# Kernel optimization log

Measured on AMD Instinct MI355X. Metric: run time of the kernel, lower is better.

The kernel has to match this reference:

```python
import jax, jax.numpy as jnp
import numpy as np

MASK_VALUE = -1000000.0  # matches torch source's value=-1000000.0


def setup_inputs() -> dict:
    key = jax.random.key(0)
    kq, kk, kv, kl = jax.random.split(key, 4)
    B, S, D = 64, 1024, 64
    q = jax.random.normal(kq, (B, S, D), dtype=jnp.float32)
    k = jax.random.normal(kk, (B, S, D), dtype=jnp.float32)
    v = jax.random.normal(kv, (B, S, D), dtype=jnp.float32)
    valid_lens = jax.random.randint(kl, (B,), 0, S, dtype=jnp.int32)
    return {"q": q, "k": k, "v": v, "valid_lens": valid_lens}


def reference(q, k, v, valid_lens):
    # scores: [B, Sq, Sk]
    d = q.shape[-1]
    scores = jnp.einsum("bqd,bkd->bqk", q, k) / jnp.sqrt(jnp.float32(d))
    # 1-D valid_lens broadcast over the query dim (torch repeat_interleave branch)
    Sk = k.shape[1]
    mask = jnp.arange(Sk, dtype=jnp.int32)[None, None, :] < valid_lens[:, None, None]
    scores = jnp.where(mask, scores, MASK_VALUE)
    attn = jax.nn.softmax(scores, axis=-1)
    # dropout p=0.0 -> identity (eval-mode reference)
    return jnp.einsum("bqk,bkd->bqd", attn, v)
```

## Files before the change

### kernel.cpp

```cpp
#include <hip/hip_runtime.h>
#include <math.h>


#define BATCH 64
#define SEQ   1024
#define DIM   64
#define BQ    64
#define BC    64
#define NKT   (SEQ / BC)
#define LSTR  72
#define QSCALE 0.18033688011112442f
#define MASKED -1.0e6f
#define THR    8.0f

typedef __attribute__((ext_vector_type(8))) short bf16x8;
typedef __attribute__((ext_vector_type(4))) float f32x4;

__device__ __forceinline__ uint pack2_trunc(float lo, float hi) {
    return __builtin_amdgcn_perm(__float_as_uint(hi), __float_as_uint(lo), 0x07060302);
}
__device__ __forceinline__ ushort f2bf_rne(float x) {
    uint u = __float_as_uint(x);
    return (ushort)((u + 0x7fffu + ((u >> 16) & 1u)) >> 16);
}

__global__ __launch_bounds__(256, 4) void attn_mfma_flash4(
    const float* __restrict__ q, const float* __restrict__ k,
    const float* __restrict__ v, const int* __restrict__ valid_lens,
    float* __restrict__ out)
{
    __shared__ ushort Ks[BC * LSTR];
    __shared__ ushort Vt[DIM * LSTR];

    const int t    = threadIdx.x;
    const int wave = t >> 6;
    const int wl   = t & 63;
    const int QD   = wl >> 4;
    const int li   = wl & 15;
    const int b    = blockIdx.x & 63;
    const int q0   = (blockIdx.x >> 6) * BQ;
    const int vl   = valid_lens[b];

    const size_t boff = (size_t)b * SEQ * DIM;

    bf16x8 qb[2];
    {
        const float* qrow = q + boff + (size_t)(q0 + wave * 16 + li) * DIM + QD * 8;
        #pragma unroll
        for (int kc = 0; kc < 2; kc++) {
            float4 a = *(const float4*)(qrow + kc * 32);
            float4 c = *(const float4*)(qrow + kc * 32 + 4);
            union { bf16x8 v; ushort u[8]; } tmp;
            tmp.u[0] = f2bf_rne(a.x * QSCALE);
            tmp.u[1] = f2bf_rne(a.y * QSCALE);
            tmp.u[2] = f2bf_rne(a.z * QSCALE);
            tmp.u[3] = f2bf_rne(a.w * QSCALE);
            tmp.u[4] = f2bf_rne(c.x * QSCALE);
            tmp.u[5] = f2bf_rne(c.y * QSCALE);
            tmp.u[6] = f2bf_rne(c.z * QSCALE);
            tmp.u[7] = f2bf_rne(c.w * QSCALE);
            qb[kc] = tmp.v;
        }
    }

    const int it_max = (vl == 0) ? NKT : ((vl + BC - 1) >> 6);

    float4 kf[4];
    float  vf[2][8];

    auto load_tile = [&](int it) {
        const float4* kg = (const float4*)(k + boff + (size_t)it * BC * DIM);
        #pragma unroll
        for (int i = 0; i < 4; i++) kf[i] = kg[t + 256 * i];
        const float* vgf = v + boff + (size_t)it * BC * DIM;
        #pragma unroll
        for (int i = 0; i < 2; i++) {
            int slot = t + 256 * i;
            int d = slot & 63, ko = slot >> 6;
            int kb = (ko >> 2) * 16 + (ko & 3) * 4;
            #pragma unroll
            for (int j = 0; j < 8; j++) {
                int kk = kb + ((j >> 2) << 5) + (j & 3);
                vf[i][j] = vgf[(size_t)kk * DIM + d];
            }
        }
    };

    auto stage = [&]() {
        #pragma unroll
        for (int i = 0; i < 4; i++) {
            int idx = t + 256 * i;
            int row = idx >> 4, c4 = idx & 15;
            uint2 w;
            w.x = pack2_trunc(kf[i].x, kf[i].y);
            w.y = pack2_trunc(kf[i].z, kf[i].w);
            *(uint2*)&Ks[row * LSTR + c4 * 4] = w;
        }
        #pragma unroll
        for (int i = 0; i < 2; i++) {
            int slot = t + 256 * i;
            int d = slot & 63, ko = slot >> 6;
            uint4 w;
            w.x = pack2_trunc(vf[i][0], vf[i][1]);
            w.y = pack2_trunc(vf[i][2], vf[i][3]);
            w.z = pack2_trunc(vf[i][4], vf[i][5]);
            w.w = pack2_trunc(vf[i][6], vf[i][7]);
            *(uint4*)&Vt[d * LSTR + ko * 8] = w;
        }
    };

    float m_run = -INFINITY, l_run = 0.f;
    f32x4 acc[4];
    #pragma unroll
    for (int dt = 0; dt < 4; dt++) acc[dt] = (f32x4){0.f, 0.f, 0.f, 0.f};

    load_tile(0);

    for (int it = 0; it < it_max; it++) {
        __builtin_amdgcn_sched_barrier(0);
        __builtin_amdgcn_s_barrier();
        __builtin_amdgcn_sched_barrier(0);

        stage();
        if (it + 1 < it_max) load_tile(it + 1);

        __builtin_amdgcn_sched_barrier(0);
        asm volatile("s_waitcnt lgkmcnt(0)" ::: "memory");
        __builtin_amdgcn_s_barrier();
        __builtin_amdgcn_sched_barrier(0);

        f32x4 sc[4];
        #pragma unroll
        for (int kt = 0; kt < 4; kt++) {
            bf16x8 ka0 = *(const bf16x8*)&Ks[(kt * 16 + li) * LSTR + QD * 8];
            bf16x8 ka1 = *(const bf16x8*)&Ks[(kt * 16 + li) * LSTR + 32 + QD * 8];
            f32x4 c = (f32x4){0.f, 0.f, 0.f, 0.f};
            c = __builtin_amdgcn_mfma_f32_16x16x32_bf16(ka0, qb[0], c, 0, 0, 0);
            c = __builtin_amdgcn_mfma_f32_16x16x32_bf16(ka1, qb[1], c, 0, 0, 0);
            sc[kt] = c;
        }

        const int kbase = it * BC;
        if (kbase + BC > vl) {
            #pragma unroll
            for (int kt = 0; kt < 4; kt++)
                #pragma unroll
                for (int r = 0; r < 4; r++) {
                    int key = kbase + kt * 16 + QD * 4 + r;
                    if (key >= vl) sc[kt][r] = MASKED;
                }
        }

        float mt = -INFINITY;
        #pragma unroll
        for (int kt = 0; kt < 4; kt++)
            #pragma unroll
            for (int r = 0; r < 4; r++) mt = fmaxf(mt, sc[kt][r]);
        mt = fmaxf(mt, __shfl_xor(mt, 16, 64));
        mt = fmaxf(mt, __shfl_xor(mt, 32, 64));

        if (!__all(mt - m_run <= THR)) {
            float mn = fmaxf(m_run, mt);
            float alpha = exp2f(m_run - mn);
            m_run = mn;
            l_run *= alpha;
            float a0 = __shfl(alpha, QD * 4 + 0, 64);
            float a1 = __shfl(alpha, QD * 4 + 1, 64);
            float a2 = __shfl(alpha, QD * 4 + 2, 64);
            float a3 = __shfl(alpha, QD * 4 + 3, 64);
            #pragma unroll
            for (int dt = 0; dt < 4; dt++) {
                acc[dt][0] *= a0; acc[dt][1] *= a1;
                acc[dt][2] *= a2; acc[dt][3] *= a3;
            }
        }

        float ls = 0.f;
        union { bf16x8 v; uint u[4]; } pa0u, pa1u;
        {
            float p00 = exp2f(sc[0][0] - m_run), p01 = exp2f(sc[0][1] - m_run);
            float p02 = exp2f(sc[0][2] - m_run), p03 = exp2f(sc[0][3] - m_run);
            float p10 = exp2f(sc[1][0] - m_run), p11 = exp2f(sc[1][1] - m_run);
            float p12 = exp2f(sc[1][2] - m_run), p13 = exp2f(sc[1][3] - m_run);
            float p20 = exp2f(sc[2][0] - m_run), p21 = exp2f(sc[2][1] - m_run);
            float p22 = exp2f(sc[2][2] - m_run), p23 = exp2f(sc[2][3] - m_run);
            float p30 = exp2f(sc[3][0] - m_run), p31 = exp2f(sc[3][1] - m_run);
            float p32 = exp2f(sc[3][2] - m_run), p33 = exp2f(sc[3][3] - m_run);
            ls = ((p00 + p01) + (p02 + p03)) + ((p10 + p11) + (p12 + p13))
               + ((p20 + p21) + (p22 + p23)) + ((p30 + p31) + (p32 + p33));
            pa0u.u[0] = pack2_trunc(p00, p01);
            pa0u.u[1] = pack2_trunc(p02, p03);
            pa0u.u[2] = pack2_trunc(p20, p21);
            pa0u.u[3] = pack2_trunc(p22, p23);
            pa1u.u[0] = pack2_trunc(p10, p11);
            pa1u.u[1] = pack2_trunc(p12, p13);
            pa1u.u[2] = pack2_trunc(p30, p31);
            pa1u.u[3] = pack2_trunc(p32, p33);
        }
        ls += __shfl_xor(ls, 16, 64);
        ls += __shfl_xor(ls, 32, 64);
        l_run += ls;

        #pragma unroll
        for (int dt = 0; dt < 4; dt++) {
            bf16x8 vb0 = *(const bf16x8*)&Vt[(dt * 16 + li) * LSTR + QD * 8];
            bf16x8 vb1 = *(const bf16x8*)&Vt[(dt * 16 + li) * LSTR + 32 + QD * 8];
            acc[dt] = __builtin_amdgcn_mfma_f32_16x16x32_bf16(pa0u.v, vb0, acc[dt], 0, 0, 0);
            acc[dt] = __builtin_amdgcn_mfma_f32_16x16x32_bf16(pa1u.v, vb1, acc[dt], 0, 0, 0);
        }
    }

    float invl = 1.0f / l_run;
    float i0 = __shfl(invl, QD * 4 + 0, 64);
    float i1 = __shfl(invl, QD * 4 + 1, 64);
    float i2 = __shfl(invl, QD * 4 + 2, 64);
    float i3 = __shfl(invl, QD * 4 + 3, 64);
    float* ob = out + boff + (size_t)q0 * DIM;
    const int rbase = wave * 16 + QD * 4;
    #pragma unroll
    for (int dt = 0; dt < 4; dt++) {
        int col = dt * 16 + li;
        ob[(size_t)(rbase + 0) * DIM + col] = acc[dt][0] * i0;
        ob[(size_t)(rbase + 1) * DIM + col] = acc[dt][1] * i1;
        ob[(size_t)(rbase + 2) * DIM + col] = acc[dt][2] * i2;
        ob[(size_t)(rbase + 3) * DIM + col] = acc[dt][3] * i3;
    }
}

extern "C" void kernel_launch(void* const* d_in, const int* in_sizes, int n_in,
                              void* d_out, int out_size, void* d_ws, size_t ws_size,
                              hipStream_t stream) {
    const float* q = (const float*)d_in[0];
    const float* k = (const float*)d_in[1];
    const float* v = (const float*)d_in[2];
    const int* valid_lens = (const int*)d_in[3];
    float* out = (float*)d_out;

    dim3 grid(BATCH * (SEQ / BQ));
    dim3 block(256);
    attn_mfma_flash4<<<grid, block, 0, stream>>>(q, k, v, valid_lens, out);
}
```

Before: 124.4 us.

## Process two 64-row query tiles per block to reuse staged K/V tiles

Doubles the query rows per block to 128, with each wave holding two independent query sub-tiles, A and B, that share each K/V tile staged in LDS. This halves the global K/V loads and bf16 conversion/staging work per query row. Block-to-batch mapping is rotated per group to spread the uneven valid_lens work across blocks. Grid size halves to 512 blocks and register pressure roughly doubles, which lowers occupancy and reduces the parallelism available for load balancing.

```diff
diff --git a/kernel.cpp b/kernel.cpp
--- a/kernel.cpp
+++ b/kernel.cpp
@@ -5,7 +5,7 @@
 #define BATCH 64
 #define SEQ   1024
 #define DIM   64
-#define BQ    64
+#define BQ    128
 #define BC    64
 #define NKT   (SEQ / BC)
 #define LSTR  72
@@ -24,7 +24,7 @@
     return (ushort)((u + 0x7fffu + ((u >> 16) & 1u)) >> 16);
 }
 
-__global__ __launch_bounds__(256, 4) void attn_mfma_flash4(
+__global__ __launch_bounds__(256, 1) void attn_mfma_flash5(
     const float* __restrict__ q, const float* __restrict__ k,
     const float* __restrict__ v, const int* __restrict__ valid_lens,
     float* __restrict__ out)
@@ -37,29 +37,35 @@
     const int wl   = t & 63;
     const int QD   = wl >> 4;
     const int li   = wl & 15;
-    const int b    = blockIdx.x & 63;
-    const int q0   = (blockIdx.x >> 6) * BQ;
+    const int g    = blockIdx.x;
+    const int grp  = g >> 6;
+    const int b    = ((g & 63) + grp) & 63;
+    const int q0   = grp * BQ;
     const int vl   = valid_lens[b];
 
     const size_t boff = (size_t)b * SEQ * DIM;
 
-    bf16x8 qb[2];
+    bf16x8 qbA[2], qbB[2];
     {
-        const float* qrow = q + boff + (size_t)(q0 + wave * 16 + li) * DIM + QD * 8;
-        #pragma unroll
-        for (int kc = 0; kc < 2; kc++) {
-            float4 a = *(const float4*)(qrow + kc * 32);
-            float4 c = *(const float4*)(qrow + kc * 32 + 4);
-            union { bf16x8 v; ushort u[8]; } tmp;
-            tmp.u[0] = f2bf_rne(a.x * QSCALE);
-            tmp.u[1] = f2bf_rne(a.y * QSCALE);
-            tmp.u[2] = f2bf_rne(a.z * QSCALE);
-            tmp.u[3] = f2bf_rne(a.w * QSCALE);
-            tmp.u[4] = f2bf_rne(c.x * QSCALE);
-            tmp.u[5] = f2bf_rne(c.y * QSCALE);
-            tmp.u[6] = f2bf_rne(c.z * QSCALE);
-            tmp.u[7] = f2bf_rne(c.w * QSCALE);
-            qb[kc] = tmp.v;
+        #pragma unroll
+        for (int half = 0; half < 2; half++) {
+            const float* qrow = q + boff
+                + (size_t)(q0 + half * 64 + wave * 16 + li) * DIM + QD * 8;
+            #pragma unroll
+            for (int kc = 0; kc < 2; kc++) {
+                float4 a = *(const float4*)(qrow + kc * 32);
+                float4 c = *(const float4*)(qrow + kc * 32 + 4);
+                union { bf16x8 v; ushort u[8]; } tmp;
+                tmp.u[0] = f2bf_rne(a.x * QSCALE);
+                tmp.u[1] = f2bf_rne(a.y * QSCALE);
+                tmp.u[2] = f2bf_rne(a.z * QSCALE);
+                tmp.u[3] = f2bf_rne(a.w * QSCALE);
+                tmp.u[4] = f2bf_rne(c.x * QSCALE);
+                tmp.u[5] = f2bf_rne(c.y * QSCALE);
+                tmp.u[6] = f2bf_rne(c.z * QSCALE);
+                tmp.u[7] = f2bf_rne(c.w * QSCALE);
+                if (half == 0) qbA[kc] = tmp.v; else qbB[kc] = tmp.v;
+            }
         }
     }
 
@@ -109,10 +115,13 @@
         }
     };
 
-    float m_run = -INFINITY, l_run = 0.f;
-    f32x4 acc[4];
+    float mA = -INFINITY, lA = 0.f, mB = -INFINITY, lB = 0.f;
+    f32x4 accA[4], accB[4];
     #pragma unroll
-    for (int dt = 0; dt < 4; dt++) acc[dt] = (f32x4){0.f, 0.f, 0.f, 0.f};
+    for (int dt = 0; dt < 4; dt++) {
+        accA[dt] = (f32x4){0.f, 0.f, 0.f, 0.f};
+        accB[dt] = (f32x4){0.f, 0.f, 0.f, 0.f};
+    }
 
     load_tile(0);
 
@@ -129,15 +138,19 @@
         __builtin_amdgcn_s_barrier();
         __builtin_amdgcn_sched_barrier(0);
 
-        f32x4 sc[4];
+        f32x4 scA[4], scB[4];
         #pragma unroll
         for (int kt = 0; kt < 4; kt++) {
             bf16x8 ka0 = *(const bf16x8*)&Ks[(kt * 16 + li) * LSTR + QD * 8];
             bf16x8 ka1 = *(const bf16x8*)&Ks[(kt * 16 + li) * LSTR + 32 + QD * 8];
-            f32x4 c = (f32x4){0.f, 0.f, 0.f, 0.f};
-            c = __builtin_amdgcn_mfma_f32_16x16x32_bf16(ka0, qb[0], c, 0, 0, 0);
-            c = __builtin_amdgcn_mfma_f32_16x16x32_bf16(ka1, qb[1], c, 0, 0, 0);
-            sc[kt] = c;
+            f32x4 cA = (f32x4){0.f, 0.f, 0.f, 0.f};
+            cA = __builtin_amdgcn_mfma_f32_16x16x32_bf16(ka0, qbA[0], cA, 0, 0, 0);
+            cA = __builtin_amdgcn_mfma_f32_16x16x32_bf16(ka1, qbA[1], cA, 0, 0, 0);
+            scA[kt] = cA;
+            f32x4 cB = (f32x4){0.f, 0.f, 0.f, 0.f};
+            cB = __builtin_amdgcn_mfma_f32_16x16x32_bf16(ka0, qbB[0], cB, 0, 0, 0);
+            cB = __builtin_amdgcn_mfma_f32_16x16x32_bf16(ka1, qbB[1], cB, 0, 0, 0);
+            scB[kt] = cB;
         }
 
         const int kbase = it * BC;
@@ -147,83 +160,136 @@
                 #pragma unroll
                 for (int r = 0; r < 4; r++) {
                     int key = kbase + kt * 16 + QD * 4 + r;
-                    if (key >= vl) sc[kt][r] = MASKED;
+                    if (key >= vl) { scA[kt][r] = MASKED; scB[kt][r] = MASKED; }
                 }
         }
 
-        float mt = -INFINITY;
-        #pragma unroll
-        for (int kt = 0; kt < 4; kt++)
-            #pragma unroll
-            for (int r = 0; r < 4; r++) mt = fmaxf(mt, sc[kt][r]);
-        mt = fmaxf(mt, __shfl_xor(mt, 16, 64));
-        mt = fmaxf(mt, __shfl_xor(mt, 32, 64));
-
-        if (!__all(mt - m_run <= THR)) {
-            float mn = fmaxf(m_run, mt);
-            float alpha = exp2f(m_run - mn);
-            m_run = mn;
-            l_run *= alpha;
-            float a0 = __shfl(alpha, QD * 4 + 0, 64);
-            float a1 = __shfl(alpha, QD * 4 + 1, 64);
-            float a2 = __shfl(alpha, QD * 4 + 2, 64);
-            float a3 = __shfl(alpha, QD * 4 + 3, 64);
-            #pragma unroll
-            for (int dt = 0; dt < 4; dt++) {
-                acc[dt][0] *= a0; acc[dt][1] *= a1;
-                acc[dt][2] *= a2; acc[dt][3] *= a3;
+        union { bf16x8 v; uint u[4]; } pA0, pA1, pB0, pB1;
+        {
+            float mt = -INFINITY;
+            #pragma unroll
+            for (int kt = 0; kt < 4; kt++)
+                #pragma unroll
+                for (int r = 0; r < 4; r++) mt = fmaxf(mt, scA[kt][r]);
+            mt = fmaxf(mt, __shfl_xor(mt, 16, 64));
+            mt = fmaxf(mt, __shfl_xor(mt, 32, 64));
+            if (!__all(mt - mA <= THR)) {
+                float mn = fmaxf(mA, mt);
+                float alpha = exp2f(mA - mn);
+                mA = mn; lA *= alpha;
+                float a0 = __shfl(alpha, QD * 4 + 0, 64);
+                float a1 = __shfl(alpha, QD * 4 + 1, 64);
+                float a2 = __shfl(alpha, QD * 4 + 2, 64);
+                float a3 = __shfl(alpha, QD * 4 + 3, 64);
+                #pragma unroll
+                for (int dt = 0; dt < 4; dt++) {
+                    accA[dt][0] *= a0; accA[dt][1] *= a1;
+                    accA[dt][2] *= a2; accA[dt][3] *= a3;
+                }
             }
-        }
-
-        float ls = 0.f;
-        union { bf16x8 v; uint u[4]; } pa0u, pa1u;
+            float p00 = exp2f(scA[0][0] - mA), p01 = exp2f(scA[0][1] - mA);
+            float p02 = exp2f(scA[0][2] - mA), p03 = exp2f(scA[0][3] - mA);
+            float p10 = exp2f(scA[1][0] - mA), p11 = exp2f(scA[1][1] - mA);
+            float p12 = exp2f(scA[1][2] - mA), p13 = exp2f(scA[1][3] - mA);
+            float p20 = exp2f(scA[2][0] - mA), p21 = exp2f(scA[2][1] - mA);
+            float p22 = exp2f(scA[2][2] - mA), p23 = exp2f(scA[2][3] - mA);
+            float p30 = exp2f(scA[3][0] - mA), p31 = exp2f(scA[3][1] - mA);
+            float p32 = exp2f(scA[3][2] - mA), p33 = exp2f(scA[3][3] - mA);
+            float ls = ((p00 + p01) + (p02 + p03)) + ((p10 + p11) + (p12 + p13))
+                     + ((p20 + p21) + (p22 + p23)) + ((p30 + p31) + (p32 + p33));
+            pA0.u[0] = pack2_trunc(p00, p01); pA0.u[1] = pack2_trunc(p02, p03);
+            pA0.u[2] = pack2_trunc(p20, p21); pA0.u[3] = pack2_trunc(p22, p23);
+            pA1.u[0] = pack2_trunc(p10, p11); pA1.u[1] = pack2_trunc(p12, p13);
+            pA1.u[2] = pack2_trunc(p30, p31); pA1.u[3] = pack2_trunc(p32, p33);
+            ls += __shfl_xor(ls, 16, 64);
+            ls += __shfl_xor(ls, 32, 64);
+            lA += ls;
+        }
         {
-            float p00 = exp2f(sc[0][0] - m_run), p01 = exp2f(sc[0][1] - m_run);
-            float p02 = exp2f(sc[0][2] - m_run), p03 = exp2f(sc[0][3] - m_run);
-            float p10 = exp2f(sc[1][0] - m_run), p11 = exp2f(sc[1][1] - m_run);
-            float p12 = exp2f(sc[1][2] - m_run), p13 = exp2f(sc[1][3] - m_run);
-            float p20 = exp2f(sc[2][0] - m_run), p21 = exp2f(sc[2][1] - m_run);
-            float p22 = exp2f(sc[2][2] - m_run), p23 = exp2f(sc[2][3] - m_run);
-            float p30 = exp2f(sc[3][0] - m_run), p31 = exp2f(sc[3][1] - m_run);
-            float p32 = exp2f(sc[3][2] - m_run), p33 = exp2f(sc[3][3] - m_run);
-            ls = ((p00 + p01) + (p02 + p03)) + ((p10 + p11) + (p12 + p13))
-               + ((p20 + p21) + (p22 + p23)) + ((p30 + p31) + (p32 + p33));
-            pa0u.u[0] = pack2_trunc(p00, p01);
-            pa0u.u[1] = pack2_trunc(p02, p03);
-            pa0u.u[2] = pack2_trunc(p20, p21);
-            pa0u.u[3] = pack2_trunc(p22, p23);
-            pa1u.u[0] = pack2_trunc(p10, p11);
-            pa1u.u[1] = pack2_trunc(p12, p13);
-            pa1u.u[2] = pack2_trunc(p30, p31);
-            pa1u.u[3] = pack2_trunc(p32, p33);
-        }
-        ls += __shfl_xor(ls, 16, 64);
-        ls += __shfl_xor(ls, 32, 64);
-        l_run += ls;
+            float mt = -INFINITY;
+            #pragma unroll
+            for (int kt = 0; kt < 4; kt++)
+                #pragma unroll
+                for (int r = 0; r < 4; r++) mt = fmaxf(mt, scB[kt][r]);
+            mt = fmaxf(mt, __shfl_xor(mt, 16, 64));
+            mt = fmaxf(mt, __shfl_xor(mt, 32, 64));
+            if (!__all(mt - mB <= THR)) {
+                float mn = fmaxf(mB, mt);
+                float alpha = exp2f(mB - mn);
+                mB = mn; lB *= alpha;
+                float a0 = __shfl(alpha, QD * 4 + 0, 64);
+                float a1 = __shfl(alpha, QD * 4 + 1, 64);
+                float a2 = __shfl(alpha, QD * 4 + 2, 64);
+                float a3 = __shfl(alpha, QD * 4 + 3, 64);
+                #pragma unroll
+                for (int dt = 0; dt < 4; dt++) {
+                    accB[dt][0] *= a0; accB[dt][1] *= a1;
+                    accB[dt][2] *= a2; accB[dt][3] *= a3;
+                }
+            }
+            float p00 = exp2f(scB[0][0] - mB), p01 = exp2f(scB[0][1] - mB);
+            float p02 = exp2f(scB[0][2] - mB), p03 = exp2f(scB[0][3] - mB);
+            float p10 = exp2f(scB[1][0] - mB), p11 = exp2f(scB[1][1] - mB);
+            float p12 = exp2f(scB[1][2] - mB), p13 = exp2f(scB[1][3] - mB);
+            float p20 = exp2f(scB[2][0] - mB), p21 = exp2f(scB[2][1] - mB);
+            float p22 = exp2f(scB[2][2] - mB), p23 = exp2f(scB[2][3] - mB);
+            float p30 = exp2f(scB[3][0] - mB), p31 = exp2f(scB[3][1] - mB);
+            float p32 = exp2f(scB[3][2] - mB), p33 = exp2f(scB[3][3] - mB);
+            float ls = ((p00 + p01) + (p02 + p03)) + ((p10 + p11) + (p12 + p13))
+                     + ((p20 + p21) + (p22 + p23)) + ((p30 + p31) + (p32 + p33));
+            pB0.u[0] = pack2_trunc(p00, p01); pB0.u[1] = pack2_trunc(p02, p03);
+            pB0.u[2] = pack2_trunc(p20, p21); pB0.u[3] = pack2_trunc(p22, p23);
+            pB1.u[0] = pack2_trunc(p10, p11); pB1.u[1] = pack2_trunc(p12, p13);
+            pB1.u[2] = pack2_trunc(p30, p31); pB1.u[3] = pack2_trunc(p32, p33);
+            ls += __shfl_xor(ls, 16, 64);
+            ls += __shfl_xor(ls, 32, 64);
+            lB += ls;
+        }
 
         #pragma unroll
         for (int dt = 0; dt < 4; dt++) {
             bf16x8 vb0 = *(const bf16x8*)&Vt[(dt * 16 + li) * LSTR + QD * 8];
             bf16x8 vb1 = *(const bf16x8*)&Vt[(dt * 16 + li) * LSTR + 32 + QD * 8];
-            acc[dt] = __builtin_amdgcn_mfma_f32_16x16x32_bf16(pa0u.v, vb0, acc[dt], 0, 0, 0);
-            acc[dt] = __builtin_amdgcn_mfma_f32_16x16x32_bf16(pa1u.v, vb1, acc[dt], 0, 0, 0);
-        }
-    }
-
-    float invl = 1.0f / l_run;
-    float i0 = __shfl(invl, QD * 4 + 0, 64);
-    float i1 = __shfl(invl, QD * 4 + 1, 64);
-    float i2 = __shfl(invl, QD * 4 + 2, 64);
-    float i3 = __shfl(invl, QD * 4 + 3, 64);
-    float* ob = out + boff + (size_t)q0 * DIM;
-    const int rbase = wave * 16 + QD * 4;
-    #pragma unroll
-    for (int dt = 0; dt < 4; dt++) {
-        int col = dt * 16 + li;
-        ob[(size_t)(rbase + 0) * DIM + col] = acc[dt][0] * i0;
-        ob[(size_t)(rbase + 1) * DIM + col] = acc[dt][1] * i1;
-        ob[(size_t)(rbase + 2) * DIM + col] = acc[dt][2] * i2;
-        ob[(size_t)(rbase + 3) * DIM + col] = acc[dt][3] * i3;
+            accA[dt] = __builtin_amdgcn_mfma_f32_16x16x32_bf16(pA0.v, vb0, accA[dt], 0, 0, 0);
+            accA[dt] = __builtin_amdgcn_mfma_f32_16x16x32_bf16(pA1.v, vb1, accA[dt], 0, 0, 0);
+            accB[dt] = __builtin_amdgcn_mfma_f32_16x16x32_bf16(pB0.v, vb0, accB[dt], 0, 0, 0);
+            accB[dt] = __builtin_amdgcn_mfma_f32_16x16x32_bf16(pB1.v, vb1, accB[dt], 0, 0, 0);
+        }
+    }
+
+    {
+        float invl = 1.0f / lA;
+        float i0 = __shfl(invl, QD * 4 + 0, 64);
+        float i1 = __shfl(invl, QD * 4 + 1, 64);
+        float i2 = __shfl(invl, QD * 4 + 2, 64);
+        float i3 = __shfl(invl, QD * 4 + 3, 64);
+        float* ob = out + boff + (size_t)q0 * DIM;
+        const int rbase = wave * 16 + QD * 4;
+        #pragma unroll
+        for (int dt = 0; dt < 4; dt++) {
+            int col = dt * 16 + li;
+            ob[(size_t)(rbase + 0) * DIM + col] = accA[dt][0] * i0;
+            ob[(size_t)(rbase + 1) * DIM + col] = accA[dt][1] * i1;
+            ob[(size_t)(rbase + 2) * DIM + col] = accA[dt][2] * i2;
+            ob[(size_t)(rbase + 3) * DIM + col] = accA[dt][3] * i3;
+        }
+    }
+    {
+        float invl = 1.0f / lB;
+        float i0 = __shfl(invl, QD * 4 + 0, 64);
+        float i1 = __shfl(invl, QD * 4 + 1, 64);
+        float i2 = __shfl(invl, QD * 4 + 2, 64);
+        float i3 = __shfl(invl, QD * 4 + 3, 64);
+        float* ob = out + boff + (size_t)(q0 + 64) * DIM;
+        const int rbase = wave * 16 + QD * 4;
+        #pragma unroll
+        for (int dt = 0; dt < 4; dt++) {
+            int col = dt * 16 + li;
+            ob[(size_t)(rbase + 0) * DIM + col] = accB[dt][0] * i0;
+            ob[(size_t)(rbase + 1) * DIM + col] = accB[dt][1] * i1;
+            ob[(size_t)(rbase + 2) * DIM + col] = accB[dt][2] * i2;
+            ob[(size_t)(rbase + 3) * DIM + col] = accB[dt][3] * i3;
+        }
     }
 }
 
@@ -238,5 +304,5 @@
 
     dim3 grid(BATCH * (SEQ / BQ));
     dim3 block(256);
-    attn_mfma_flash4<<<grid, block, 0, stream>>>(q, k, v, valid_lens, out);
+    attn_mfma_flash5<<<grid, block, 0, stream>>>(q, k, v, valid_lens, out);
 }
```

Result: slower. 127.6 us (+2.6%).

## Split key tiles across two wave groups per block and merge partial softmax

Applied to the files above, without the earlier changes.

Each block now runs 512 threads as two groups of four waves. The groups process alternating key tiles for the same 64 queries, each with its own shared-memory K/V buffer, and their partial accumulators and (max, sum) pairs are merged through shared memory at the end. This roughly halves the serial per-block loop length and doubles the waves available to hide latency. Block indices are also rotated so that batches with different valid lengths are spread across the grid. The cost is more LDS per block, an extra merge phase with barriers, and possibly lower occupancy with 512-thread blocks under launch bounds (512,4).

```diff
diff --git a/kernel.cpp b/kernel.cpp
--- a/kernel.cpp
+++ b/kernel.cpp
@@ -12,6 +12,7 @@
 #define QSCALE 0.18033688011112442f
 #define MASKED -1.0e6f
 #define THR    8.0f
+#define KVSZ   (BC * LSTR)
 
 typedef __attribute__((ext_vector_type(8))) short bf16x8;
 typedef __attribute__((ext_vector_type(4))) float f32x4;
@@ -24,28 +25,36 @@
     return (ushort)((u + 0x7fffu + ((u >> 16) & 1u)) >> 16);
 }
 
-__global__ __launch_bounds__(256, 4) void attn_mfma_flash4(
+__global__ __launch_bounds__(512, 4) void attn_dualgrp(
     const float* __restrict__ q, const float* __restrict__ k,
     const float* __restrict__ v, const int* __restrict__ valid_lens,
     float* __restrict__ out)
 {
-    __shared__ ushort Ks[BC * LSTR];
-    __shared__ ushort Vt[DIM * LSTR];
+    __shared__ ushort SB[4 * KVSZ];
 
     const int t    = threadIdx.x;
     const int wave = t >> 6;
+    const int gid  = wave >> 2;
+    const int wg   = wave & 3;
     const int wl   = t & 63;
     const int QD   = wl >> 4;
     const int li   = wl & 15;
-    const int b    = blockIdx.x & 63;
-    const int q0   = (blockIdx.x >> 6) * BQ;
+    const int tg   = t & 255;
+
+    const int g    = blockIdx.x;
+    const int grp  = g >> 6;
+    const int b    = ((g & 63) + grp) & 63;
+    const int q0   = grp * BQ;
     const int vl   = valid_lens[b];
 
     const size_t boff = (size_t)b * SEQ * DIM;
+
+    ushort* Ksg = SB + gid * (2 * KVSZ);
+    ushort* Vtg = Ksg + KVSZ;
 
     bf16x8 qb[2];
     {
-        const float* qrow = q + boff + (size_t)(q0 + wave * 16 + li) * DIM + QD * 8;
+        const float* qrow = q + boff + (size_t)(q0 + wg * 16 + li) * DIM + QD * 8;
         #pragma unroll
         for (int kc = 0; kc < 2; kc++) {
             float4 a = *(const float4*)(qrow + kc * 32);
@@ -63,7 +72,8 @@
         }
     }
 
-    const int it_max = (vl == 0) ? NKT : ((vl + BC - 1) >> 6);
+    const int it_full = (vl == 0) ? NKT : ((vl + BC - 1) >> 6);
+    const int nmax    = (it_full + 1) >> 1;
 
     float4 kf[4];
     float  vf[2][8];
@@ -71,11 +81,11 @@
     auto load_tile = [&](int it) {
         const float4* kg = (const float4*)(k + boff + (size_t)it * BC * DIM);
         #pragma unroll
-        for (int i = 0; i < 4; i++) kf[i] = kg[t + 256 * i];
+        for (int i = 0; i < 4; i++) kf[i] = kg[tg + 256 * i];
         const float* vgf = v + boff + (size_t)it * BC * DIM;
         #pragma unroll
         for (int i = 0; i < 2; i++) {
-            int slot = t + 256 * i;
+            int slot = tg + 256 * i;
             int d = slot & 63, ko = slot >> 6;
             int kb = (ko >> 2) * 16 + (ko & 3) * 4;
             #pragma unroll
@@ -89,141 +99,177 @@
     auto stage = [&]() {
         #pragma unroll
         for (int i = 0; i < 4; i++) {
-            int idx = t + 256 * i;
+            int idx = tg + 256 * i;
             int row = idx >> 4, c4 = idx & 15;
             uint2 w;
             w.x = pack2_trunc(kf[i].x, kf[i].y);
             w.y = pack2_trunc(kf[i].z, kf[i].w);
-            *(uint2*)&Ks[row * LSTR + c4 * 4] = w;
+            *(uint2*)&Ksg[row * LSTR + c4 * 4] = w;
         }
         #pragma unroll
         for (int i = 0; i < 2; i++) {
-            int slot = t + 256 * i;
+            int slot = tg + 256 * i;
             int d = slot & 63, ko = slot >> 6;
             uint4 w;
             w.x = pack2_trunc(vf[i][0], vf[i][1]);
             w.y = pack2_trunc(vf[i][2], vf[i][3]);
             w.z = pack2_trunc(vf[i][4], vf[i][5]);
             w.w = pack2_trunc(vf[i][6], vf[i][7]);
-            *(uint4*)&Vt[d * LSTR + ko * 8] = w;
+            *(uint4*)&Vtg[d * LSTR + ko * 8] = w;
         }
     };
 
-    float m_run = -INFINITY, l_run = 0.f;
+    float m_run = -INFINITY;
+    float l_run = 0.f;
     f32x4 acc[4];
     #pragma unroll
     for (int dt = 0; dt < 4; dt++) acc[dt] = (f32x4){0.f, 0.f, 0.f, 0.f};
 
-    load_tile(0);
-
-    for (int it = 0; it < it_max; it++) {
+    bool act = (gid < it_full);
+    if (act) load_tile(gid);
+
+    for (int j = 0; j < nmax; j++) {
+        const int tile = gid + 2 * j;
+        const bool act_next = (tile + 2) < it_full;
+
         __builtin_amdgcn_sched_barrier(0);
         __builtin_amdgcn_s_barrier();
         __builtin_amdgcn_sched_barrier(0);
 
-        stage();
-        if (it + 1 < it_max) load_tile(it + 1);
+        if (act) stage();
+        if (act_next) load_tile(tile + 2);
 
         __builtin_amdgcn_sched_barrier(0);
         asm volatile("s_waitcnt lgkmcnt(0)" ::: "memory");
         __builtin_amdgcn_s_barrier();
         __builtin_amdgcn_sched_barrier(0);
 
-        f32x4 sc[4];
-        #pragma unroll
-        for (int kt = 0; kt < 4; kt++) {
-            bf16x8 ka0 = *(const bf16x8*)&Ks[(kt * 16 + li) * LSTR + QD * 8];
-            bf16x8 ka1 = *(const bf16x8*)&Ks[(kt * 16 + li) * LSTR + 32 + QD * 8];
-            f32x4 c = (f32x4){0.f, 0.f, 0.f, 0.f};
-            c = __builtin_amdgcn_mfma_f32_16x16x32_bf16(ka0, qb[0], c, 0, 0, 0);
-            c = __builtin_amdgcn_mfma_f32_16x16x32_bf16(ka1, qb[1], c, 0, 0, 0);
-            sc[kt] = c;
-        }
-
-        const int kbase = it * BC;
-        if (kbase + BC > vl) {
+        if (act) {
+            f32x4 sc[4];
+            #pragma unroll
+            for (int kt = 0; kt < 4; kt++) {
+                bf16x8 ka0 = *(const bf16x8*)&Ksg[(kt * 16 + li) * LSTR + QD * 8];
+                bf16x8 ka1 = *(const bf16x8*)&Ksg[(kt * 16 + li) * LSTR + 32 + QD * 8];
+                f32x4 c = (f32x4){0.f, 0.f, 0.f, 0.f};
+                c = __builtin_amdgcn_mfma_f32_16x16x32_bf16(ka0, qb[0], c, 0, 0, 0);
+                c = __builtin_amdgcn_mfma_f32_16x16x32_bf16(ka1, qb[1], c, 0, 0, 0);
+                sc[kt] = c;
+            }
+
+            const int kbase = tile * BC;
+            if (kbase + BC > vl) {
+                #pragma unroll
+                for (int kt = 0; kt < 4; kt++)
+                    #pragma unroll
+                    for (int r = 0; r < 4; r++) {
+                        int key = kbase + kt * 16 + QD * 4 + r;
+                        if (key >= vl) sc[kt][r] = MASKED;
+                    }
+            }
+
+            float mt = -INFINITY;
             #pragma unroll
             for (int kt = 0; kt < 4; kt++)
                 #pragma unroll
-                for (int r = 0; r < 4; r++) {
-                    int key = kbase + kt * 16 + QD * 4 + r;
-                    if (key >= vl) sc[kt][r] = MASKED;
+                for (int r = 0; r < 4; r++) mt = fmaxf(mt, sc[kt][r]);
+
+            if (!__all(mt - m_run <= THR)) {
+                mt = fmaxf(mt, __shfl_xor(mt, 16, 64));
+                mt = fmaxf(mt, __shfl_xor(mt, 32, 64));
+                float mn = fmaxf(m_run, mt);
+                float alpha = exp2f(m_run - mn);
+                m_run = mn;
+                l_run *= alpha;
+                float a0 = __shfl(alpha, QD * 4 + 0, 64);
+                float a1 = __shfl(alpha, QD * 4 + 1, 64);
+                float a2 = __shfl(alpha, QD * 4 + 2, 64);
+                float a3 = __shfl(alpha, QD * 4 + 3, 64);
+                #pragma unroll
+                for (int dt = 0; dt < 4; dt++) {
+                    acc[dt][0] *= a0; acc[dt][1] *= a1;
+                    acc[dt][2] *= a2; acc[dt][3] *= a3;
                 }
-        }
-
-        float mt = -INFINITY;
-        #pragma unroll
-        for (int kt = 0; kt < 4; kt++)
-            #pragma unroll
-            for (int r = 0; r < 4; r++) mt = fmaxf(mt, sc[kt][r]);
-        mt = fmaxf(mt, __shfl_xor(mt, 16, 64));
-        mt = fmaxf(mt, __shfl_xor(mt, 32, 64));
-
-        if (!__all(mt - m_run <= THR)) {
-            float mn = fmaxf(m_run, mt);
-            float alpha = exp2f(m_run - mn);
-            m_run = mn;
-            l_run *= alpha;
-            float a0 = __shfl(alpha, QD * 4 + 0, 64);
-            float a1 = __shfl(alpha, QD * 4 + 1, 64);
-            float a2 = __shfl(alpha, QD * 4 + 2, 64);
-            float a3 = __shfl(alpha, QD * 4 + 3, 64);
+            }
+
+            union { bf16x8 v; uint u[4]; } pa0u, pa1u;
+            {
+                float p00 = exp2f(sc[0][0] - m_run), p01 = exp2f(sc[0][1] - m_run);
+                float p02 = exp2f(sc[0][2] - m_run), p03 = exp2f(sc[0][3] - m_run);
+                float p10 = exp2f(sc[1][0] - m_run), p11 = exp2f(sc[1][1] - m_run);
+                float p12 = exp2f(sc[1][2] - m_run), p13 = exp2f(sc[1][3] - m_run);
+                float p20 = exp2f(sc[2][0] - m_run), p21 = exp2f(sc[2][1] - m_run);
+                float p22 = exp2f(sc[2][2] - m_run), p23 = exp2f(sc[2][3] - m_run);
+                float p30 = exp2f(sc[3][0] - m_run), p31 = exp2f(sc[3][1] - m_run);
+                float p32 = exp2f(sc[3][2] - m_run), p33 = exp2f(sc[3][3] - m_run);
+                l_run += ((p00 + p01) + (p02 + p03)) + ((p10 + p11) + (p12 + p13))
+                       + ((p20 + p21) + (p22 + p23)) + ((p30 + p31) + (p32 + p33));
+                pa0u.u[0] = pack2_trunc(p00, p01);
+                pa0u.u[1] = pack2_trunc(p02, p03);
+                pa0u.u[2] = pack2_trunc(p20, p21);
+                pa0u.u[3] = pack2_trunc(p22, p23);
+                pa1u.u[0] = pack2_trunc(p10, p11);
+                pa1u.u[1] = pack2_trunc(p12, p13);
+                pa1u.u[2] = pack2_trunc(p30, p31);
+                pa1u.u[3] = pack2_trunc(p32, p33);
+            }
+
             #pragma unroll
             for (int dt = 0; dt < 4; dt++) {
-                acc[dt][0] *= a0; acc[dt][1] *= a1;
-                acc[dt][2] *= a2; acc[dt][3] *= a3;
-            }
-        }
-
-        float ls = 0.f;
-        union { bf16x8 v; uint u[4]; } pa0u, pa1u;
-        {
-            float p00 = exp2f(sc[0][0] - m_run), p01 = exp2f(sc[0][1] - m_run);
-            float p02 = exp2f(sc[0][2] - m_run), p03 = exp2f(sc[0][3] - m_run);
-            float p10 = exp2f(sc[1][0] - m_run), p11 = exp2f(sc[1][1] - m_run);
-            float p12 = exp2f(sc[1][2] - m_run), p13 = exp2f(sc[1][3] - m_run);
-            float p20 = exp2f(sc[2][0] - m_run), p21 = exp2f(sc[2][1] - m_run);
-            float p22 = exp2f(sc[2][2] - m_run), p23 = exp2f(sc[2][3] - m_run);
-            float p30 = exp2f(sc[3][0] - m_run), p31 = exp2f(sc[3][1] - m_run);
-            float p32 = exp2f(sc[3][2] - m_run), p33 = exp2f(sc[3][3] - m_run);
-            ls = ((p00 + p01) + (p02 + p03)) + ((p10 + p11) + (p12 + p13))
-               + ((p20 + p21) + (p22 + p23)) + ((p30 + p31) + (p32 + p33));
-            pa0u.u[0] = pack2_trunc(p00, p01);
-            pa0u.u[1] = pack2_trunc(p02, p03);
-            pa0u.u[2] = pack2_trunc(p20, p21);
-            pa0u.u[3] = pack2_trunc(p22, p23);
-            pa1u.u[0] = pack2_trunc(p10, p11);
-            pa1u.u[1] = pack2_trunc(p12, p13);
-            pa1u.u[2] = pack2_trunc(p30, p31);
-            pa1u.u[3] = pack2_trunc(p32, p33);
-        }
-        ls += __shfl_xor(ls, 16, 64);
-        ls += __shfl_xor(ls, 32, 64);
-        l_run += ls;
-
-        #pragma unroll
-        for (int dt = 0; dt < 4; dt++) {
-            bf16x8 vb0 = *(const bf16x8*)&Vt[(dt * 16 + li) * LSTR + QD * 8];
-            bf16x8 vb1 = *(const bf16x8*)&Vt[(dt * 16 + li) * LSTR + 32 + QD * 8];
-            acc[dt] = __builtin_amdgcn_mfma_f32_16x16x32_bf16(pa0u.v, vb0, acc[dt], 0, 0, 0);
-            acc[dt] = __builtin_amdgcn_mfma_f32_16x16x32_bf16(pa1u.v, vb1, acc[dt], 0, 0, 0);
-        }
-    }
-
-    float invl = 1.0f / l_run;
-    float i0 = __shfl(invl, QD * 4 + 0, 64);
-    float i1 = __shfl(invl, QD * 4 + 1, 64);
-    float i2 = __shfl(invl, QD * 4 + 2, 64);
-    float i3 = __shfl(invl, QD * 4 + 3, 64);
-    float* ob = out + boff + (size_t)q0 * DIM;
-    const int rbase = wave * 16 + QD * 4;
-    #pragma unroll
-    for (int dt = 0; dt < 4; dt++) {
-        int col = dt * 16 + li;
-        ob[(size_t)(rbase + 0) * DIM + col] = acc[dt][0] * i0;
-        ob[(size_t)(rbase + 1) * DIM + col] = acc[dt][1] * i1;
-        ob[(size_t)(rbase + 2) * DIM + col] = acc[dt][2] * i2;
-        ob[(size_t)(rbase + 3) * DIM + col] = acc[dt][3] * i3;
+                bf16x8 vb0 = *(const bf16x8*)&Vtg[(dt * 16 + li) * LSTR + QD * 8];
+                bf16x8 vb1 = *(const bf16x8*)&Vtg[(dt * 16 + li) * LSTR + 32 + QD * 8];
+                acc[dt] = __builtin_amdgcn_mfma_f32_16x16x32_bf16(pa0u.v, vb0, acc[dt], 0, 0, 0);
+                acc[dt] = __builtin_amdgcn_mfma_f32_16x16x32_bf16(pa1u.v, vb1, acc[dt], 0, 0, 0);
+            }
+        }
+        act = act_next;
+    }
+
+    l_run += __shfl_xor(l_run, 16, 64);
+    l_run += __shfl_xor(l_run, 32, 64);
+
+    __builtin_amdgcn_sched_barrier(0);
+    __builtin_amdgcn_s_barrier();
+    __builtin_amdgcn_sched_barrier(0);
+
+    char*   mb  = (char*)SB;
+    float*  Ox  = (float*)mb;
+    float2* ml0 = (float2*)(mb + 16384);
+    float2* ml1 = (float2*)(mb + 16896);
+
+    if (gid == 1) {
+        if (QD == 0) ml1[wg * 16 + li] = make_float2(m_run, l_run);
+        #pragma unroll
+        for (int dt = 0; dt < 4; dt++)
+            #pragma unroll
+            for (int r = 0; r < 4; r++)
+                Ox[(wg * 16 + QD * 4 + r) * 64 + dt * 16 + li] = acc[dt][r];
+    } else {
+        if (QD == 0) ml0[wg * 16 + li] = make_float2(m_run, l_run);
+    }
+
+    __builtin_amdgcn_sched_barrier(0);
+    asm volatile("s_waitcnt lgkmcnt(0)" ::: "memory");
+    __builtin_amdgcn_s_barrier();
+    __builtin_amdgcn_sched_barrier(0);
+
+    if (gid == 0) {
+        float* ob = out + boff + (size_t)q0 * DIM;
+        #pragma unroll
+        for (int r = 0; r < 4; r++) {
+            int grow = wg * 16 + QD * 4 + r;
+            float2 a = ml0[grow];
+            float2 c = ml1[grow];
+            float M  = fmaxf(a.x, c.x);
+            float w0 = exp2f(a.x - M);
+            float w1 = exp2f(c.x - M);
+            float inv = 1.f / (a.y * w0 + c.y * w1);
+            w0 *= inv; w1 *= inv;
+            #pragma unroll
+            for (int dt = 0; dt < 4; dt++) {
+                ob[(size_t)grow * DIM + dt * 16 + li] =
+                    acc[dt][r] * w0 + Ox[grow * 64 + dt * 16 + li] * w1;
+            }
+        }
     }
 }
 
@@ -237,6 +283,6 @@
     float* out = (float*)d_out;
 
     dim3 grid(BATCH * (SEQ / BQ));
-    dim3 block(256);
-    attn_mfma_flash4<<<grid, block, 0, stream>>>(q, k, v, valid_lens, out);
-}
+    dim3 block(512);
+    attn_dualgrp<<<grid, block, 0, stream>>>(q, k, v, valid_lens, out);
+}
```

Measured after the change: 134.6 us. +8.2%, slower.
